# Optimization experiments

Measured on AMD Instinct MI355X. Metric: run time of the kernel, lower is better.

The kernel has to match this reference:

```python
import jax, jax.numpy as jnp
import numpy as np

B, S, D = 4, 4096, 1024
EPS_LN = 1e-5
EPS_REC = 1e-8


def _layernorm(x, g, b):
    mu = jnp.mean(x, axis=-1, keepdims=True)
    var = jnp.mean((x - mu) ** 2, axis=-1, keepdims=True)
    return (x - mu) * jax.lax.rsqrt(var + EPS_LN) * g + b


def setup_inputs() -> dict:
    key = jax.random.key(0)
    ks = jax.random.split(key, 8)
    scale = 1.0 / np.sqrt(D)
    return {
        "x": jax.random.normal(ks[0], (B, S, D), dtype=jnp.float32),
        "x_prev": jax.random.normal(ks[1], (B, S, D), dtype=jnp.float32),
        "mu": jnp.float32(0.5),
        "decay_w": jax.random.uniform(ks[2], (D, 1), jnp.float32, -scale, scale),
        "decay_b": jnp.zeros((1,), jnp.float32),
        "ln1_g": jnp.ones((D,), jnp.float32),
        "ln1_b": jnp.zeros((D,), jnp.float32),
        "Wr_w": jax.random.uniform(ks[3], (D, D), jnp.float32, -scale, scale),
        "Wr_b": jnp.zeros((D,), jnp.float32),
        "Wv_w": jax.random.uniform(ks[4], (D, D), jnp.float32, -scale, scale),
        "Wv_b": jnp.zeros((D,), jnp.float32),
        "ln2_g": jnp.ones((D,), jnp.float32),
        "ln2_b": jnp.zeros((D,), jnp.float32),
    }


def reference(x, x_prev, mu, decay_w, decay_b, ln1_g, ln1_b,
              Wr_w, Wr_b, Wv_w, Wv_b, ln2_g, ln2_b):
    # Shift (token-mix by scalar mu)
    shifted = mu * x + (1.0 - mu) * x_prev  # [B,S,D]

    # SequenceMergingSeq with C = V = W = shifted
    decay = jax.nn.sigmoid(jnp.einsum("bsd,do->bso", shifted, decay_w) + decay_b)  # [B,S,1]
    e = jnp.exp(shifted)                       # [B,S,D]
    ea = jnp.sum(e, axis=-1, keepdims=True)    # [B,S,1]
    ev = e * shifted                           # [B,S,D]

    def step(carry, inp):
        a, b = carry
        d_t, ea_t, ev_t = inp
        a = d_t * a + ea_t            # [B,1]
        b = d_t * b + ev_t            # [B,D]
        return (a, b), b / (a + EPS_REC)

    init = (jnp.zeros((B, 1), shifted.dtype), jnp.zeros((B, D), shifted.dtype))
    xs = (jnp.swapaxes(decay, 0, 1), jnp.swapaxes(ea, 0, 1), jnp.swapaxes(ev, 0, 1))
    _, out_sbd = jax.lax.scan(step, init, xs)  # [S,B,D]
    merged = _layernorm(jnp.swapaxes(out_sbd, 0, 1), ln1_g, ln1_b)  # [B,S,D]

    # StateCoupling
    gate = jax.nn.sigmoid(jnp.einsum("bsd,ed->bse", merged, Wr_w) + Wr_b)
    value = jnp.einsum("bsd,ed->bse", merged, Wv_w) + Wv_b
    coupled = _layernorm(gate * value, ln2_g, ln2_b)

    return shifted + coupled
```

## Files before the change

### kernel.cpp

```cpp
#include <hip/hip_runtime.h>

#define BATCH 4
#define SEQ   4096
#define DIM   1024
#define NCH   512
#define CHK   8
#define NROWS (BATCH*SEQ)
#define NKT   32

typedef __attribute__((ext_vector_type(4))) float f32x4;
typedef __attribute__((ext_vector_type(8))) short shortx8;
typedef __attribute__((ext_vector_type(4))) short shortx4;

static __device__ __forceinline__ unsigned short f2bf(float f){
    unsigned int u = __float_as_uint(f);
    u += 0x7FFFu + ((u >> 16) & 1u);
    return (unsigned short)(u >> 16);
}
static __device__ __forceinline__ float bf2f(unsigned short h){
    return __uint_as_float(((unsigned int)h) << 16);
}
static __device__ __forceinline__ float sigmoidf_fast(float x){
    return 1.0f / (1.0f + __expf(-x));
}
static __device__ __forceinline__ shortx4 pack4(f32x4 s){
    shortx4 o;
    o.x = (short)f2bf(s.x); o.y = (short)f2bf(s.y);
    o.z = (short)f2bf(s.z); o.w = (short)f2bf(s.w);
    return o;
}
static __device__ __forceinline__ f32x4 unpack4(shortx4 s){
    f32x4 o;
    o.x = bf2f((unsigned short)s.x); o.y = bf2f((unsigned short)s.y);
    o.z = bf2f((unsigned short)s.z); o.w = bf2f((unsigned short)s.w);
    return o;
}

__global__ __launch_bounds__(256) void k_shift_scan(
    const float* __restrict__ X, const float* __restrict__ XP,
    const float* __restrict__ mu_p, const float* __restrict__ dw,
    const float* __restrict__ db_p,
    const float* __restrict__ Wr, const float* __restrict__ Wv,
    unsigned short* __restrict__ Wcat,
    unsigned short* __restrict__ shifted,
    unsigned short* __restrict__ b_local, float* __restrict__ a_local,
    float* __restrict__ cumP)
{
    const int tid  = threadIdx.x;

    if (blockIdx.x >= 512){
        const int pb = blockIdx.x - 512;
        #pragma unroll 4
        for (int i = 0; i < 32; ++i){
            const int n = pb*32 + i;
            const int grp = n >> 5, r = n & 31;
            const float* src = (r < 16) ? (Wr + (size_t)(grp*16 + r)*DIM)
                                        : (Wv + (size_t)(grp*16 + (r-16))*DIM);
            f32x4 v = reinterpret_cast<const f32x4*>(src)[tid];
            reinterpret_cast<shortx4*>(Wcat)[n*256 + tid] = pack4(v);
        }
        return;
    }

    const int lane = tid & 63;
    const int wid  = tid >> 6;
    const int cid  = blockIdx.x*4 + wid;
    const int batch = cid >> 9;
    const int chunk = cid & (NCH-1);
    const int row0  = batch*SEQ + chunk*CHK;

    const float mu = mu_p[0];
    const float om = 1.0f - mu;
    const float db = db_p[0];

    const f32x4* dwv = reinterpret_cast<const f32x4*>(dw);
    const f32x4 w0 = dwv[lane], w1 = dwv[64+lane], w2 = dwv[128+lane], w3 = dwv[192+lane];

    f32x4 b0 = {0,0,0,0}, b1 = {0,0,0,0}, b2 = {0,0,0,0}, b3 = {0,0,0,0};
    float a_run = 0.f, cp = 1.f;

    const f32x4* Xv  = reinterpret_cast<const f32x4*>(X);
    const f32x4* XPv = reinterpret_cast<const f32x4*>(XP);
    shortx4* BL = reinterpret_cast<shortx4*>(b_local);
    shortx4* SH = reinterpret_cast<shortx4*>(shifted);

    for (int r = 0; r < CHK; ++r){
        const int row = row0 + r;
        const int rb  = row*(DIM/4);

        f32x4 x0 = Xv[rb+lane],     x1 = Xv[rb+64+lane],
              x2 = Xv[rb+128+lane], x3 = Xv[rb+192+lane];
        f32x4 p0 = XPv[rb+lane],     p1 = XPv[rb+64+lane],
              p2 = XPv[rb+128+lane], p3 = XPv[rb+192+lane];
        f32x4 s0 = mu*x0 + om*p0, s1 = mu*x1 + om*p1;
        f32x4 s2 = mu*x2 + om*p2, s3 = mu*x3 + om*p3;

        SH[rb+lane]     = pack4(s0);
        SH[rb+64+lane]  = pack4(s1);
        SH[rb+128+lane] = pack4(s2);
        SH[rb+192+lane] = pack4(s3);

        float dot = s0.x*w0.x + s0.y*w0.y + s0.z*w0.z + s0.w*w0.w
                  + s1.x*w1.x + s1.y*w1.y + s1.z*w1.z + s1.w*w1.w
                  + s2.x*w2.x + s2.y*w2.y + s2.z*w2.z + s2.w*w2.w
                  + s3.x*w3.x + s3.y*w3.y + s3.z*w3.z + s3.w*w3.w;

        f32x4 e0, e1, e2, e3;
        e0.x=__expf(s0.x); e0.y=__expf(s0.y); e0.z=__expf(s0.z); e0.w=__expf(s0.w);
        e1.x=__expf(s1.x); e1.y=__expf(s1.y); e1.z=__expf(s1.z); e1.w=__expf(s1.w);
        e2.x=__expf(s2.x); e2.y=__expf(s2.y); e2.z=__expf(s2.z); e2.w=__expf(s2.w);
        e3.x=__expf(s3.x); e3.y=__expf(s3.y); e3.z=__expf(s3.z); e3.w=__expf(s3.w);
        float ea = e0.x+e0.y+e0.z+e0.w + e1.x+e1.y+e1.z+e1.w
                 + e2.x+e2.y+e2.z+e2.w + e3.x+e3.y+e3.z+e3.w;

        #pragma unroll
        for (int off = 1; off < 64; off <<= 1){
            dot += __shfl_xor(dot, off, 64);
            ea  += __shfl_xor(ea,  off, 64);
        }

        const float dt = sigmoidf_fast(dot + db);
        a_run = dt*a_run + ea;
        cp   *= dt;
        b0 = dt*b0 + e0*s0;  b1 = dt*b1 + e1*s1;
        b2 = dt*b2 + e2*s2;  b3 = dt*b3 + e3*s3;

        BL[rb+lane]     = pack4(b0);
        BL[rb+64+lane]  = pack4(b1);
        BL[rb+128+lane] = pack4(b2);
        BL[rb+192+lane] = pack4(b3);
        if (lane == 0){ a_local[row] = a_run; cumP[row] = cp; }
    }
}

__global__ __launch_bounds__(64) void k_combine(
    const unsigned short* __restrict__ b_local, const float* __restrict__ a_local,
    const float* __restrict__ cumP,
    float* __restrict__ carryA, unsigned short* __restrict__ carryB)
{
    const int batch = blockIdx.x >> 2;
    const int dseg  = blockIdx.x & 3;
    const int tid = threadIdx.x;
    const int d0 = dseg*256 + tid*4;

    __shared__ float sP[NCH], sA[NCH];
    for (int c = tid; c < NCH; c += 64){
        const int er = batch*SEQ + c*CHK + (CHK-1);
        sP[c] = cumP[er];
        sA[c] = a_local[er];
    }
    __syncthreads();

    const unsigned short* bl = b_local + (size_t)batch*SEQ*DIM + d0;
    unsigned short* cB = carryB + (size_t)batch*NCH*DIM + d0;
    const bool wA = (dseg == 0 && tid == 0);
    float* cAp = carryA + batch*NCH;

    shortx4 pf[16];
    #pragma unroll
    for (int i = 0; i < 16; ++i)
        pf[i] = *reinterpret_cast<const shortx4*>(bl + (i*CHK + CHK-1)*DIM);

    f32x4 cb = {0,0,0,0};
    float ca = 0.f;

    for (int cc = 0; cc < NCH; cc += 16){
        const bool more = (cc + 16 < NCH);
        #pragma unroll
        for (int k = 0; k < 16; ++k){
            const int c = cc + k;
            f32x4 v = unpack4(pf[k]);
            if (more)
                pf[k] = *reinterpret_cast<const shortx4*>(bl + ((c+16)*CHK + CHK-1)*DIM);
            *reinterpret_cast<shortx4*>(cB + (size_t)c*DIM) = pack4(cb);
            if (wA) cAp[c] = ca;
            const float p = sP[c];
            cb = p*cb + v;
            ca = p*ca + sA[c];
        }
    }
}

static __device__ __forceinline__ void block_reduce2(float& s, float& s2, float* red, int tid){
    #pragma unroll
    for (int off = 1; off < 64; off <<= 1){
        s  += __shfl_xor(s,  off, 64);
        s2 += __shfl_xor(s2, off, 64);
    }
    const int wid = tid >> 6, lane = tid & 63;
    if (lane == 0){ red[wid] = s; red[4+wid] = s2; }
    __syncthreads();
    s  = red[0]+red[1]+red[2]+red[3];
    s2 = red[4]+red[5]+red[6]+red[7];
}

__global__ __launch_bounds__(256) void k_fix_ln1(
    const unsigned short* __restrict__ b_local, const float* __restrict__ a_local,
    const float* __restrict__ cumP, const float* __restrict__ carryA,
    const unsigned short* __restrict__ carryB,
    const float* __restrict__ g1, const float* __restrict__ bb1,
    unsigned short* __restrict__ merged)
{
    const int row = blockIdx.x;
    const int batch = row >> 12;
    const int t = row & (SEQ-1);
    const int c = t >> 3;
    const int tid = threadIdx.x;

    const float cpv = cumP[row];
    const float a = a_local[row] + cpv * carryA[batch*NCH + c];
    const float inv_a = 1.0f / (a + 1e-8f);

    f32x4 bl = unpack4(reinterpret_cast<const shortx4*>(b_local)[row*256 + tid]);
    f32x4 cb = unpack4(reinterpret_cast<const shortx4*>(carryB)[(batch*NCH + c)*256 + tid]);
    f32x4 o = (bl + cpv*cb) * inv_a;

    float s  = o.x+o.y+o.z+o.w;
    float s2 = o.x*o.x + o.y*o.y + o.z*o.z + o.w*o.w;
    __shared__ float red[8];
    block_reduce2(s, s2, red, tid);

    const float mean = s * (1.0f/DIM);
    const float rstd = rsqrtf(s2*(1.0f/DIM) - mean*mean + 1e-5f);
    f32x4 gg = reinterpret_cast<const f32x4*>(g1)[tid];
    f32x4 bb = reinterpret_cast<const f32x4*>(bb1)[tid];
    f32x4 m = (o - mean)*rstd*gg + bb;
    reinterpret_cast<shortx4*>(merged)[row*256 + tid] = pack4(m);
}

typedef __attribute__((address_space(3))) unsigned int lds_uint;
typedef __attribute__((address_space(1))) unsigned int glob_uint;
static __device__ __forceinline__ void gload16(const unsigned short* g, char* l){
    __builtin_amdgcn_global_load_lds((const glob_uint*)g, (lds_uint*)l, 16, 0, 0);
}
#define SBAR() do { __builtin_amdgcn_sched_barrier(0); __builtin_amdgcn_s_barrier(); __builtin_amdgcn_sched_barrier(0); } while(0)
#define LDSE 136

__global__ __launch_bounds__(512, 2) void k_gemm(
    const unsigned short* __restrict__ A,
    const unsigned short* __restrict__ Bt,
    const float* __restrict__ rbias, const float* __restrict__ vbias,
    unsigned short* __restrict__ gv)
{
    __shared__ __align__(16) char lds[131072];
    const int tid  = threadIdx.x;
    const int lane = tid & 63;
    const int wid  = tid >> 6;
    const int wm   = wid >> 2;
    const int wn   = wid & 3;

    const int bid  = blockIdx.x;
    const int wgid = (bid & 7)*64 + (bid >> 3);
    const int mt = wgid >> 3, nt = wgid & 7;
    const int m0 = mt*256, n0 = nt*256;

    const int sr  = lane >> 2;
    const int scg = (lane & 3) ^ ((lane >> 5) << 1);
    const unsigned short* gA = A  + (size_t)(m0 + wid*32 + sr)*DIM + scg*8;
    const unsigned short* gB = Bt + (size_t)(n0 + wid*32 + sr)*DIM + scg*8;

    const int fr = lane & 15, fq = lane >> 4;
    const int soff = fr*64 + ((fq*16) ^ ((fr & 8) ? 32 : 0));

    f32x4 acc[8][4];
    #pragma unroll
    for (int i = 0; i < 8; ++i)
        #pragma unroll
        for (int j = 0; j < 4; ++j) acc[i][j] = (f32x4){0,0,0,0};

    auto STAGE_A = [&](int tk){
        char* dst = &lds[(tk & 3)*32768 + wid*2048];
        const unsigned short* s0 = gA + tk*32;
        gload16(s0,          dst);
        gload16(s0 + 16*DIM, dst + 1024);
    };
    auto STAGE_B = [&](int tk){
        char* dst = &lds[(tk & 3)*32768 + 16384 + wid*2048];
        const unsigned short* s0 = gB + tk*32;
        gload16(s0,          dst);
        gload16(s0 + 16*DIM, dst + 1024);
    };

    STAGE_A(0); STAGE_B(0);
    STAGE_A(1); STAGE_B(1);
    STAGE_A(2); STAGE_B(2);
    asm volatile("s_waitcnt vmcnt(8)" ::: "memory");
    SBAR();

    for (int t = 0; t < NKT; ++t){
        const char* bufA = &lds[(t & 3)*32768];
        const char* bufB = bufA + 16384;

        if (t + 3 < NKT){ STAGE_A(t + 3); STAGE_B(t + 3); }

        shortx8 af0[4], af1[4], bf[4];
        #pragma unroll
        for (int mf = 0; mf < 4; ++mf)
            af0[mf] = *reinterpret_cast<const shortx8*>(bufA + (wm*8 + mf)*1024 + soff);
        #pragma unroll
        for (int nf = 0; nf < 4; ++nf)
            bf[nf] = *reinterpret_cast<const shortx8*>(bufB + (wn*4 + nf)*1024 + soff);
        __builtin_amdgcn_sched_barrier(0);
        #pragma unroll
        for (int mf = 0; mf < 4; ++mf)
            af1[mf] = *reinterpret_cast<const shortx8*>(bufA + (wm*8 + mf + 4)*1024 + soff);

        asm volatile("s_waitcnt lgkmcnt(4)" ::: "memory");
        __builtin_amdgcn_sched_barrier(0);
        __builtin_amdgcn_s_setprio(1);
        #pragma unroll
        for (int mf = 0; mf < 4; ++mf)
            #pragma unroll
            for (int nf = 0; nf < 4; ++nf)
                acc[mf][nf] = __builtin_amdgcn_mfma_f32_16x16x32_bf16(af0[mf], bf[nf], acc[mf][nf], 0, 0, 0);
        __builtin_amdgcn_s_setprio(0);

        asm volatile("s_waitcnt lgkmcnt(0)" ::: "memory");
        __builtin_amdgcn_sched_barrier(0);
        __builtin_amdgcn_s_setprio(1);
        #pragma unroll
        for (int mf = 0; mf < 4; ++mf)
            #pragma unroll
            for (int nf = 0; nf < 4; ++nf)
                acc[mf+4][nf] = __builtin_amdgcn_mfma_f32_16x16x32_bf16(af1[mf], bf[nf], acc[mf+4][nf], 0, 0, 0);
        __builtin_amdgcn_s_setprio(0);

        if (t <= NKT - 4)      asm volatile("s_waitcnt vmcnt(8)" ::: "memory");
        else if (t == NKT - 3) asm volatile("s_waitcnt vmcnt(4)" ::: "memory");
        else                   asm volatile("s_waitcnt vmcnt(0)" ::: "memory");
        SBAR();
    }

    __syncthreads();
    unsigned short* ep = reinterpret_cast<unsigned short*>(lds);
    #pragma unroll
    for (int pr = 0; pr < 2; ++pr){
        const int el = wn*32 + pr*16 + fr;
        const float rbe = rbias[nt*128 + el];
        const float vbe = vbias[nt*128 + el];
        #pragma unroll
        for (int mf = 0; mf < 8; ++mf){
            const int rbase = wm*128 + mf*16 + fq*4;
            f32x4 ga = acc[mf][2*pr], va = acc[mf][2*pr+1];
            #pragma unroll
            for (int q = 0; q < 4; ++q){
                const float g = sigmoidf_fast(ga[q] + rbe);
                ep[(rbase + q)*LDSE + el] = f2bf(g*(va[q] + vbe));
            }
        }
    }
    __syncthreads();
    #pragma unroll
    for (int p = 0; p < 8; ++p){
        const int r  = p*32 + (tid >> 4);
        const int c8 = tid & 15;
        shortx8 val = *reinterpret_cast<const shortx8*>(&ep[r*LDSE + c8*8]);
        *reinterpret_cast<shortx8*>(&gv[(size_t)(m0 + r)*DIM + nt*128 + c8*8]) = val;
    }
}

__global__ __launch_bounds__(256) void k_ln2_res(
    const unsigned short* __restrict__ gvb, const unsigned short* __restrict__ shifted,
    const float* __restrict__ g2, const float* __restrict__ b2,
    float* __restrict__ out)
{
    const int row = blockIdx.x, tid = threadIdx.x;
    const int idx = row*256 + tid;
    f32x4 v = unpack4(reinterpret_cast<const shortx4*>(gvb)[idx]);
    float s  = v.x+v.y+v.z+v.w;
    float s2 = v.x*v.x + v.y*v.y + v.z*v.z + v.w*v.w;
    __shared__ float red[8];
    block_reduce2(s, s2, red, tid);
    const float mean = s * (1.0f/DIM);
    const float rstd = rsqrtf(s2*(1.0f/DIM) - mean*mean + 1e-5f);
    f32x4 gg = reinterpret_cast<const f32x4*>(g2)[tid];
    f32x4 bb = reinterpret_cast<const f32x4*>(b2)[tid];
    f32x4 nv = (v - mean)*rstd*gg + bb;
    f32x4 sh = unpack4(reinterpret_cast<const shortx4*>(shifted)[idx]);
    reinterpret_cast<f32x4*>(out)[idx] = sh + nv;
}

extern "C" void kernel_launch(void* const* d_in, const int* in_sizes, int n_in,
                              void* d_out, int out_size, void* d_ws, size_t ws_size,
                              hipStream_t stream)
{
    (void)in_sizes; (void)n_in; (void)out_size; (void)ws_size;
    const float* x     = (const float*)d_in[0];
    const float* xprev = (const float*)d_in[1];
    const float* mu    = (const float*)d_in[2];
    const float* dw    = (const float*)d_in[3];
    const float* db    = (const float*)d_in[4];
    const float* ln1g  = (const float*)d_in[5];
    const float* ln1b  = (const float*)d_in[6];
    const float* Wr    = (const float*)d_in[7];
    const float* Wrb   = (const float*)d_in[8];
    const float* Wv    = (const float*)d_in[9];
    const float* Wvb   = (const float*)d_in[10];
    const float* ln2g  = (const float*)d_in[11];
    const float* ln2b  = (const float*)d_in[12];
    float* out = (float*)d_out;

    char* ws = (char*)d_ws;
    size_t off = 0;
    auto alloc = [&](size_t bytes) -> void* {
        void* p = ws + off;
        off += (bytes + 255) & ~(size_t)255;
        return p;
    };
    unsigned short* shifted = (unsigned short*)alloc((size_t)NROWS*DIM*2);
    unsigned short* b_local = (unsigned short*)alloc((size_t)NROWS*DIM*2);
    unsigned short* merged  = (unsigned short*)alloc((size_t)NROWS*DIM*2);
    unsigned short* carryB  = (unsigned short*)alloc((size_t)BATCH*NCH*DIM*2);
    unsigned short* Wcat    = (unsigned short*)alloc((size_t)2048*1024*2);
    float* a_local          = (float*)alloc((size_t)NROWS*4);
    float* cumP             = (float*)alloc((size_t)NROWS*4);
    float* carryA           = (float*)alloc((size_t)BATCH*NCH*4);
    unsigned short* gvbuf   = b_local;

    hipLaunchKernelGGL(k_shift_scan, dim3(576),   dim3(256), 0, stream,
                       x, xprev, mu, dw, db, Wr, Wv, Wcat, shifted, b_local, a_local, cumP);
    hipLaunchKernelGGL(k_combine,    dim3(16),    dim3(64),  0, stream,
                       b_local, a_local, cumP, carryA, carryB);
    hipLaunchKernelGGL(k_fix_ln1,    dim3(16384), dim3(256), 0, stream,
                       b_local, a_local, cumP, carryA, carryB, ln1g, ln1b, merged);
    hipLaunchKernelGGL(k_gemm,       dim3(512),   dim3(512), 0, stream,
                       merged, Wcat, Wrb, Wvb, gvbuf);
    hipLaunchKernelGGL(k_ln2_res,    dim3(16384), dim3(256), 0, stream,
                       gvbuf, shifted, ln2g, ln2b, out);
}
```

Measured before the change: 215.8 us.

## Restructure GEMM into 64-wide K double-buffered quadrant pipeline; warp-per-row layernorms

The GEMM main loop changes from a 4-stage ring of 32-wide K tiles to a 2-buffer scheme with 64-wide K tiles. Each K step is split into four quadrant MFMA phases, each interleaved with staging of the next tile's pieces, which is meant to cut barriers per K element and overlap global loads with compute. Both layernorm kernels now assign one wavefront per row and reduce with shuffles only, removing the LDS reduction and __syncthreads. The new GEMM schedule relies on precise vmcnt accounting, so a wrong count could create races, and it adds more barriers per iteration.

```diff
diff --git a/kernel.cpp b/kernel.cpp
--- a/kernel.cpp
+++ b/kernel.cpp
@@ -6,7 +6,7 @@
 #define NCH   512
 #define CHK   8
 #define NROWS (BATCH*SEQ)
-#define NKT   32
+#define NTG   16
 
 typedef __attribute__((ext_vector_type(4))) float f32x4;
 typedef __attribute__((ext_vector_type(8))) short shortx8;
@@ -181,19 +181,6 @@
     }
 }
 
-static __device__ __forceinline__ void block_reduce2(float& s, float& s2, float* red, int tid){
-    #pragma unroll
-    for (int off = 1; off < 64; off <<= 1){
-        s  += __shfl_xor(s,  off, 64);
-        s2 += __shfl_xor(s2, off, 64);
-    }
-    const int wid = tid >> 6, lane = tid & 63;
-    if (lane == 0){ red[wid] = s; red[4+wid] = s2; }
-    __syncthreads();
-    s  = red[0]+red[1]+red[2]+red[3];
-    s2 = red[4]+red[5]+red[6]+red[7];
-}
-
 __global__ __launch_bounds__(256) void k_fix_ln1(
     const unsigned short* __restrict__ b_local, const float* __restrict__ a_local,
     const float* __restrict__ cumP, const float* __restrict__ carryA,
@@ -201,31 +188,43 @@
     const float* __restrict__ g1, const float* __restrict__ bb1,
     unsigned short* __restrict__ merged)
 {
-    const int row = blockIdx.x;
+    const int tid = threadIdx.x, lane = tid & 63, wid = tid >> 6;
+    const int row = blockIdx.x*4 + wid;
     const int batch = row >> 12;
-    const int t = row & (SEQ-1);
-    const int c = t >> 3;
-    const int tid = threadIdx.x;
+    const int c = (row & (SEQ-1)) >> 3;
 
     const float cpv = cumP[row];
     const float a = a_local[row] + cpv * carryA[batch*NCH + c];
     const float inv_a = 1.0f / (a + 1e-8f);
 
-    f32x4 bl = unpack4(reinterpret_cast<const shortx4*>(b_local)[row*256 + tid]);
-    f32x4 cb = unpack4(reinterpret_cast<const shortx4*>(carryB)[(batch*NCH + c)*256 + tid]);
-    f32x4 o = (bl + cpv*cb) * inv_a;
-
-    float s  = o.x+o.y+o.z+o.w;
-    float s2 = o.x*o.x + o.y*o.y + o.z*o.z + o.w*o.w;
-    __shared__ float red[8];
-    block_reduce2(s, s2, red, tid);
-
+    const shortx4* BL = reinterpret_cast<const shortx4*>(b_local) + (size_t)row*256;
+    const shortx4* CB = reinterpret_cast<const shortx4*>(carryB) + (size_t)(batch*NCH + c)*256;
+
+    f32x4 o[4];
+    float s = 0.f, s2 = 0.f;
+    #pragma unroll
+    for (int j = 0; j < 4; ++j){
+        f32x4 bl = unpack4(BL[j*64 + lane]);
+        f32x4 cb = unpack4(CB[j*64 + lane]);
+        f32x4 v = (bl + cpv*cb) * inv_a;
+        o[j] = v;
+        s  += v.x+v.y+v.z+v.w;
+        s2 += v.x*v.x + v.y*v.y + v.z*v.z + v.w*v.w;
+    }
+    #pragma unroll
+    for (int off = 1; off < 64; off <<= 1){
+        s  += __shfl_xor(s,  off, 64);
+        s2 += __shfl_xor(s2, off, 64);
+    }
     const float mean = s * (1.0f/DIM);
     const float rstd = rsqrtf(s2*(1.0f/DIM) - mean*mean + 1e-5f);
-    f32x4 gg = reinterpret_cast<const f32x4*>(g1)[tid];
-    f32x4 bb = reinterpret_cast<const f32x4*>(bb1)[tid];
-    f32x4 m = (o - mean)*rstd*gg + bb;
-    reinterpret_cast<shortx4*>(merged)[row*256 + tid] = pack4(m);
+    shortx4* MG = reinterpret_cast<shortx4*>(merged) + (size_t)row*256;
+    #pragma unroll
+    for (int j = 0; j < 4; ++j){
+        f32x4 gg = reinterpret_cast<const f32x4*>(g1)[j*64 + lane];
+        f32x4 bb = reinterpret_cast<const f32x4*>(bb1)[j*64 + lane];
+        MG[j*64 + lane] = pack4((o[j] - mean)*rstd*gg + bb);
+    }
 }
 
 typedef __attribute__((address_space(3))) unsigned int lds_uint;
@@ -234,6 +233,8 @@
     __builtin_amdgcn_global_load_lds((const glob_uint*)g, (lds_uint*)l, 16, 0, 0);
 }
 #define SBAR() do { __builtin_amdgcn_sched_barrier(0); __builtin_amdgcn_s_barrier(); __builtin_amdgcn_sched_barrier(0); } while(0)
+#define LGKM0() do { asm volatile("s_waitcnt lgkmcnt(0)" ::: "memory"); __builtin_amdgcn_sched_barrier(0); } while(0)
+#define VMC(n)  asm volatile("s_waitcnt vmcnt(" #n ")" ::: "memory")
 #define LDSE 136
 
 __global__ __launch_bounds__(512, 2) void k_gemm(
@@ -246,106 +247,126 @@
     const int tid  = threadIdx.x;
     const int lane = tid & 63;
     const int wid  = tid >> 6;
-    const int wm   = wid >> 2;
-    const int wn   = wid & 3;
+    const int wqm  = wid >> 2;
+    const int wqn  = wid & 3;
 
     const int bid  = blockIdx.x;
     const int wgid = (bid & 7)*64 + (bid >> 3);
     const int mt = wgid >> 3, nt = wgid & 7;
     const int m0 = mt*256, n0 = nt*256;
 
-    const int sr  = lane >> 2;
-    const int scg = (lane & 3) ^ ((lane >> 5) << 1);
-    const unsigned short* gA = A  + (size_t)(m0 + wid*32 + sr)*DIM + scg*8;
-    const unsigned short* gB = Bt + (size_t)(n0 + wid*32 + sr)*DIM + scg*8;
+    const int rin = lane >> 2;
+    const int scg = (lane & 3) ^ (((lane >> 5) & 1) << 1);
+    const unsigned short* gA = A  + (size_t)(m0 + wid*16 + rin)*DIM + scg*8;
+    const unsigned short* gB = Bt + (size_t)(n0 + wid*16 + rin)*DIM + scg*8;
 
     const int fr = lane & 15, fq = lane >> 4;
     const int soff = fr*64 + ((fq*16) ^ ((fr & 8) ? 32 : 0));
 
-    f32x4 acc[8][4];
-    #pragma unroll
-    for (int i = 0; i < 8; ++i)
+    f32x4 acc0[8], acc1[8], acc2[8], acc3[8];
+    #pragma unroll
+    for (int i = 0; i < 8; ++i){
+        acc0[i] = (f32x4){0,0,0,0}; acc1[i] = (f32x4){0,0,0,0};
+        acc2[i] = (f32x4){0,0,0,0}; acc3[i] = (f32x4){0,0,0,0};
+    }
+
+    auto STAGE = [&](int Tk, int piece){
+        const int isA = (piece == 0 || piece == 3);
+        const int h   = (piece >= 2) ? 1 : 0;
+        char* dst = lds + (Tk & 1)*65536 + (isA ? 0 : 32768) + h*16384 + wid*2048;
+        const unsigned short* s = (isA ? gA : gB) + (size_t)(h*128)*DIM + Tk*64;
+        gload16(s,      dst);
+        gload16(s + 32, dst + 1024);
+    };
+
+    shortx8 aA[8], bB0[4], bB1[4];
+    auto LOAD_A = [&](const char* base){
         #pragma unroll
-        for (int j = 0; j < 4; ++j) acc[i][j] = (f32x4){0,0,0,0};
-
-    auto STAGE_A = [&](int tk){
-        char* dst = &lds[(tk & 3)*32768 + wid*2048];
-        const unsigned short* s0 = gA + tk*32;
-        gload16(s0,          dst);
-        gload16(s0 + 16*DIM, dst + 1024);
+        for (int rf = 0; rf < 4; ++rf)
+            #pragma unroll
+            for (int kb = 0; kb < 2; ++kb)
+                aA[rf*2+kb] = *reinterpret_cast<const shortx8*>(
+                    base + (wqm*4 + rf)*2048 + kb*1024 + soff);
     };
-    auto STAGE_B = [&](int tk){
-        char* dst = &lds[(tk & 3)*32768 + 16384 + wid*2048];
-        const unsigned short* s0 = gB + tk*32;
-        gload16(s0,          dst);
-        gload16(s0 + 16*DIM, dst + 1024);
+    auto LOAD_B = [&](const char* base, shortx8* dst){
+        #pragma unroll
+        for (int cf = 0; cf < 2; ++cf)
+            #pragma unroll
+            for (int kb = 0; kb < 2; ++kb)
+                dst[cf*2+kb] = *reinterpret_cast<const shortx8*>(
+                    base + (wqn*2 + cf)*2048 + kb*1024 + soff);
     };
 
-    STAGE_A(0); STAGE_B(0);
-    STAGE_A(1); STAGE_B(1);
-    STAGE_A(2); STAGE_B(2);
-    asm volatile("s_waitcnt vmcnt(8)" ::: "memory");
+    #define MFMA16(ACC, BX)                                                     \
+        __builtin_amdgcn_s_setprio(1);                                          \
+        _Pragma("unroll")                                                       \
+        for (int rf = 0; rf < 4; ++rf)                                          \
+            _Pragma("unroll")                                                   \
+            for (int cf = 0; cf < 2; ++cf){                                     \
+                ACC[rf*2+cf] = __builtin_amdgcn_mfma_f32_16x16x32_bf16(         \
+                    aA[rf*2+0], BX[cf*2+0], ACC[rf*2+cf], 0,0,0);               \
+                ACC[rf*2+cf] = __builtin_amdgcn_mfma_f32_16x16x32_bf16(         \
+                    aA[rf*2+1], BX[cf*2+1], ACC[rf*2+cf], 0,0,0);               \
+            }                                                                   \
+        __builtin_amdgcn_s_setprio(0);
+
+    STAGE(0,0); STAGE(0,1); STAGE(0,2); STAGE(0,3);
+    VMC(4);
     SBAR();
 
-    for (int t = 0; t < NKT; ++t){
-        const char* bufA = &lds[(t & 3)*32768];
-        const char* bufB = bufA + 16384;
-
-        if (t + 3 < NKT){ STAGE_A(t + 3); STAGE_B(t + 3); }
-
-        shortx8 af0[4], af1[4], bf[4];
-        #pragma unroll
-        for (int mf = 0; mf < 4; ++mf)
-            af0[mf] = *reinterpret_cast<const shortx8*>(bufA + (wm*8 + mf)*1024 + soff);
-        #pragma unroll
-        for (int nf = 0; nf < 4; ++nf)
-            bf[nf] = *reinterpret_cast<const shortx8*>(bufB + (wn*4 + nf)*1024 + soff);
-        __builtin_amdgcn_sched_barrier(0);
-        #pragma unroll
-        for (int mf = 0; mf < 4; ++mf)
-            af1[mf] = *reinterpret_cast<const shortx8*>(bufA + (wm*8 + mf + 4)*1024 + soff);
-
-        asm volatile("s_waitcnt lgkmcnt(4)" ::: "memory");
-        __builtin_amdgcn_sched_barrier(0);
-        __builtin_amdgcn_s_setprio(1);
-        #pragma unroll
-        for (int mf = 0; mf < 4; ++mf)
-            #pragma unroll
-            for (int nf = 0; nf < 4; ++nf)
-                acc[mf][nf] = __builtin_amdgcn_mfma_f32_16x16x32_bf16(af0[mf], bf[nf], acc[mf][nf], 0, 0, 0);
-        __builtin_amdgcn_s_setprio(0);
-
-        asm volatile("s_waitcnt lgkmcnt(0)" ::: "memory");
-        __builtin_amdgcn_sched_barrier(0);
-        __builtin_amdgcn_s_setprio(1);
-        #pragma unroll
-        for (int mf = 0; mf < 4; ++mf)
-            #pragma unroll
-            for (int nf = 0; nf < 4; ++nf)
-                acc[mf+4][nf] = __builtin_amdgcn_mfma_f32_16x16x32_bf16(af1[mf], bf[nf], acc[mf+4][nf], 0, 0, 0);
-        __builtin_amdgcn_s_setprio(0);
-
-        if (t <= NKT - 4)      asm volatile("s_waitcnt vmcnt(8)" ::: "memory");
-        else if (t == NKT - 3) asm volatile("s_waitcnt vmcnt(4)" ::: "memory");
-        else                   asm volatile("s_waitcnt vmcnt(0)" ::: "memory");
+    for (int T = 0; T < NTG; ++T){
+        const char* cb = lds + (T & 1)*65536;
+        const bool hn = (T + 1 < NTG);
+
+        LOAD_A(cb);
+        LOAD_B(cb + 32768, bB0);
+        if (hn) STAGE(T+1, 0);
+        if (hn) { VMC(4); } else { VMC(2); }
+        SBAR();
+        LGKM0();
+        MFMA16(acc0, bB0);
+        SBAR();
+
+        LOAD_B(cb + 49152, bB1);
+        if (hn) STAGE(T+1, 1);
+        if (hn) { VMC(4); } else { VMC(0); }
+        SBAR();
+        LGKM0();
+        MFMA16(acc1, bB1);
+        SBAR();
+
+        LOAD_A(cb + 16384);
+        if (hn) STAGE(T+1, 2);
+        if (hn) { VMC(4); }
+        SBAR();
+        LGKM0();
+        MFMA16(acc3, bB1);
+        SBAR();
+
+        if (hn) STAGE(T+1, 3);
+        if (hn) { VMC(4); }
+        SBAR();
+        MFMA16(acc2, bB0);
         SBAR();
     }
 
     __syncthreads();
     unsigned short* ep = reinterpret_cast<unsigned short*>(lds);
     #pragma unroll
-    for (int pr = 0; pr < 2; ++pr){
-        const int el = wn*32 + pr*16 + fr;
+    for (int q = 0; q < 4; ++q){
+        const f32x4* ac = (q==0) ? acc0 : (q==1) ? acc1 : (q==2) ? acc2 : acc3;
+        const int QM = q >> 1, QN = q & 1;
+        const int el = QN*64 + wqn*16 + fr;
         const float rbe = rbias[nt*128 + el];
         const float vbe = vbias[nt*128 + el];
         #pragma unroll
-        for (int mf = 0; mf < 8; ++mf){
-            const int rbase = wm*128 + mf*16 + fq*4;
-            f32x4 ga = acc[mf][2*pr], va = acc[mf][2*pr+1];
+        for (int rf = 0; rf < 4; ++rf){
+            const int rbase = QM*128 + wqm*64 + rf*16 + fq*4;
+            f32x4 ga = ac[rf*2+0], va = ac[rf*2+1];
             #pragma unroll
-            for (int q = 0; q < 4; ++q){
-                const float g = sigmoidf_fast(ga[q] + rbe);
-                ep[(rbase + q)*LDSE + el] = f2bf(g*(va[q] + vbe));
+            for (int qq = 0; qq < 4; ++qq){
+                const float g = sigmoidf_fast(ga[qq] + rbe);
+                ep[(rbase + qq)*LDSE + el] = f2bf(g*(va[qq] + vbe));
             }
         }
     }
@@ -357,6 +378,7 @@
         shortx8 val = *reinterpret_cast<const shortx8*>(&ep[r*LDSE + c8*8]);
         *reinterpret_cast<shortx8*>(&gv[(size_t)(m0 + r)*DIM + nt*128 + c8*8]) = val;
     }
+    #undef MFMA16
 }
 
 __global__ __launch_bounds__(256) void k_ln2_res(
@@ -364,20 +386,36 @@
     const float* __restrict__ g2, const float* __restrict__ b2,
     float* __restrict__ out)
 {
-    const int row = blockIdx.x, tid = threadIdx.x;
-    const int idx = row*256 + tid;
-    f32x4 v = unpack4(reinterpret_cast<const shortx4*>(gvb)[idx]);
-    float s  = v.x+v.y+v.z+v.w;
-    float s2 = v.x*v.x + v.y*v.y + v.z*v.z + v.w*v.w;
-    __shared__ float red[8];
-    block_reduce2(s, s2, red, tid);
+    const int tid = threadIdx.x, lane = tid & 63, wid = tid >> 6;
+    const int row = blockIdx.x*4 + wid;
+
+    const shortx4* GV = reinterpret_cast<const shortx4*>(gvb) + (size_t)row*256;
+    const shortx4* SH = reinterpret_cast<const shortx4*>(shifted) + (size_t)row*256;
+
+    f32x4 v[4];
+    float s = 0.f, s2 = 0.f;
+    #pragma unroll
+    for (int j = 0; j < 4; ++j){
+        f32x4 x = unpack4(GV[j*64 + lane]);
+        v[j] = x;
+        s  += x.x+x.y+x.z+x.w;
+        s2 += x.x*x.x + x.y*x.y + x.z*x.z + x.w*x.w;
+    }
+    #pragma unroll
+    for (int off = 1; off < 64; off <<= 1){
+        s  += __shfl_xor(s,  off, 64);
+        s2 += __shfl_xor(s2, off, 64);
+    }
     const float mean = s * (1.0f/DIM);
     const float rstd = rsqrtf(s2*(1.0f/DIM) - mean*mean + 1e-5f);
-    f32x4 gg = reinterpret_cast<const f32x4*>(g2)[tid];
-    f32x4 bb = reinterpret_cast<const f32x4*>(b2)[tid];
-    f32x4 nv = (v - mean)*rstd*gg + bb;
-    f32x4 sh = unpack4(reinterpret_cast<const shortx4*>(shifted)[idx]);
-    reinterpret_cast<f32x4*>(out)[idx] = sh + nv;
+    f32x4* O = reinterpret_cast<f32x4*>(out) + (size_t)row*256;
+    #pragma unroll
+    for (int j = 0; j < 4; ++j){
+        f32x4 gg = reinterpret_cast<const f32x4*>(g2)[j*64 + lane];
+        f32x4 bb = reinterpret_cast<const f32x4*>(b2)[j*64 + lane];
+        f32x4 sh = unpack4(SH[j*64 + lane]);
+        O[j*64 + lane] = sh + (v[j] - mean)*rstd*gg + bb;
+    }
 }
 
 extern "C" void kernel_launch(void* const* d_in, const int* in_sizes, int n_in,
@@ -417,14 +455,14 @@
     float* carryA           = (float*)alloc((size_t)BATCH*NCH*4);
     unsigned short* gvbuf   = b_local;
 
-    hipLaunchKernelGGL(k_shift_scan, dim3(576),   dim3(256), 0, stream,
+    hipLaunchKernelGGL(k_shift_scan, dim3(576),  dim3(256), 0, stream,
                        x, xprev, mu, dw, db, Wr, Wv, Wcat, shifted, b_local, a_local, cumP);
-    hipLaunchKernelGGL(k_combine,    dim3(16),    dim3(64),  0, stream,
+    hipLaunchKernelGGL(k_combine,    dim3(16),   dim3(64),  0, stream,
                        b_local, a_local, cumP, carryA, carryB);
-    hipLaunchKernelGGL(k_fix_ln1,    dim3(16384), dim3(256), 0, stream,
+    hipLaunchKernelGGL(k_fix_ln1,    dim3(4096), dim3(256), 0, stream,
                        b_local, a_local, cumP, carryA, carryB, ln1g, ln1b, merged);
-    hipLaunchKernelGGL(k_gemm,       dim3(512),   dim3(512), 0, stream,
+    hipLaunchKernelGGL(k_gemm,       dim3(512),  dim3(512), 0, stream,
                        merged, Wcat, Wrb, Wvb, gvbuf);
-    hipLaunchKernelGGL(k_ln2_res,    dim3(16384), dim3(256), 0, stream,
+    hipLaunchKernelGGL(k_ln2_res,    dim3(4096), dim3(256), 0, stream,
                        gvbuf, shifted, ln2g, ln2b, out);
 }
```

After: 206.0 us. 4.5% less time.
